# Kernel optimization log

Measured on AMD Instinct MI355X. Metric: run time of the kernel, lower is better.

## Reference

```python
import jax, jax.numpy as jnp
import numpy as np
import math

D_MODEL = 1024
NUM_HEADS = 16
D_KV = 64
INNER = NUM_HEADS * D_KV
NUM_BUCKETS = 32
MAX_DISTANCE = 128


def _relative_position_bucket(relative_position, num_buckets=NUM_BUCKETS, max_distance=MAX_DISTANCE):
    # bidirectional T5 bucketing
    n = -relative_position
    num_buckets = num_buckets // 2
    ret = (n < 0).astype(jnp.int32) * num_buckets
    n = jnp.abs(n)
    max_exact = num_buckets // 2
    is_small = n < max_exact
    n_safe = jnp.maximum(n, 1).astype(jnp.float32)  # avoid log(0); masked by is_small
    val_if_large = max_exact + (
        jnp.log(n_safe / max_exact) / math.log(max_distance / max_exact) * (num_buckets - max_exact)
    ).astype(jnp.int32)
    val_if_large = jnp.minimum(val_if_large, num_buckets - 1)
    return jnp.where(is_small, n, val_if_large) + ret


def _position_bias(rel_emb, q_len, k_len):
    ctx = jnp.arange(q_len)[:, None]
    mem = jnp.arange(k_len)[None, :]
    buckets = _relative_position_bucket(mem - ctx)          # [q, k]
    values = rel_emb[buckets]                               # [q, k, H]
    return jnp.transpose(values, (2, 0, 1))[None]           # [1, H, q, k]


def setup_inputs() -> dict:
    key = jax.random.key(0)
    ks = jax.random.split(key, 6)
    B, S = 2, 2048
    scale = 1.0 / math.sqrt(D_MODEL)
    return {
        "hidden_states": jax.random.normal(ks[0], (B, S, D_MODEL), dtype=jnp.float32),
        "mask": jnp.zeros((B, 1, 1, S), dtype=jnp.float32),
        "Wq": jax.random.normal(ks[1], (D_MODEL, INNER), dtype=jnp.float32) * scale,
        "Wk": jax.random.normal(ks[2], (D_MODEL, INNER), dtype=jnp.float32) * scale,
        "Wv": jax.random.normal(ks[3], (D_MODEL, INNER), dtype=jnp.float32) * scale,
        "Wo": jax.random.normal(ks[4], (INNER, D_MODEL), dtype=jnp.float32) * scale,
        "rel_emb": jax.random.normal(ks[5], (NUM_BUCKETS, NUM_HEADS), dtype=jnp.float32),
    }


def reference(hidden_states, mask, Wq, Wk, Wv, Wo, rel_emb):
    B, S, _ = hidden_states.shape
    def split_heads(x):
        return jnp.transpose(x.reshape(B, -1, NUM_HEADS, D_KV), (0, 2, 1, 3))  # [B,H,S,d]
    q = split_heads(hidden_states @ Wq)
    k = split_heads(hidden_states @ Wk)
    v = split_heads(hidden_states @ Wv)
    scores = jnp.einsum("bhqd,bhkd->bhqk", q, k)            # unscaled, T5-style
    position_bias = _position_bias(rel_emb, S, S)           # [1,H,S,S]
    scores = scores + position_bias + mask
    attn = jax.nn.softmax(scores, axis=-1)
    context = jnp.einsum("bhqk,bhkd->bhqd", attn, v)
    context = jnp.transpose(context, (0, 2, 1, 3)).reshape(B, S, INNER)
    output = context @ Wo
    return output, position_bias
```

## Files before the change

### kernel.cpp

```cpp
#include <hip/hip_runtime.h>
#include <cstdint>

#define AS1 __attribute__((address_space(1)))
#define AS3 __attribute__((address_space(3)))

typedef _Float16 half8 __attribute__((ext_vector_type(8)));
typedef _Float16 half4_t __attribute__((ext_vector_type(4)));
typedef float v4f __attribute__((ext_vector_type(4)));

__device__ __forceinline__ void async_ld16(const void* g, void* l) {
  __builtin_amdgcn_global_load_lds((const AS1 uint32_t*)g, (AS3 uint32_t*)l, 16, 0, 0);
}

__device__ __forceinline__ int t5_bucket(int delta) {
  int n = -delta;
  int ret = 0;
  if (n < 0) { ret = 16; n = -n; }
  if (n < 8) return n + ret;
  if (n >= 91) return 15 + ret;
  if ((n & (n - 1)) == 0) {
    int l = 31 - __clz(n);
    int v = 2 + 2 * l;
    return (v > 15 ? 15 : v) + ret;
  }
  int v = 8 + (int)(logf((float)n * 0.125f) * (8.0f / logf(16.0f)));
  return (v > 15 ? 15 : v) + ret;
}

__global__ void k_cvt(const float* __restrict__ src, _Float16* __restrict__ dst) {
  int t = blockIdx.x * 256 + threadIdx.x;
  float4 f = ((const float4*)src)[t];
  half4_t h = {(_Float16)f.x, (_Float16)f.y, (_Float16)f.z, (_Float16)f.w};
  ((half4_t*)dst)[t] = h;
}

__global__ void k_wt_all(const float* __restrict__ Wq, const float* __restrict__ Wk,
                         const float* __restrict__ Wv, const float* __restrict__ Wo,
                         _Float16* __restrict__ wqkvT, _Float16* __restrict__ woT) {
  __shared__ float tile[32][33];
  const int z = blockIdx.z;
  const float* src = (z == 0) ? Wq : (z == 1) ? Wk : (z == 2) ? Wv : Wo;
  _Float16* dst = (z < 3) ? (wqkvT + ((size_t)z << 20)) : woT;
  int tx = threadIdx.x, ty = threadIdx.y;
  int bx = blockIdx.x * 32, by = blockIdx.y * 32;
#pragma unroll
  for (int i = 0; i < 32; i += 8)
    tile[ty + i][tx] = src[(size_t)(by + ty + i) * 1024 + bx + tx];
  __syncthreads();
#pragma unroll
  for (int i = 0; i < 32; i += 8)
    dst[(size_t)(bx + ty + i) * 1024 + by + tx] = (_Float16)tile[tx][ty + i];
}

__global__ __launch_bounds__(256, 2) void k_gemm_qkv_bias(
    const _Float16* __restrict__ A, const _Float16* __restrict__ BT,
    _Float16* __restrict__ qkv, _Float16* __restrict__ vT,
    const float* __restrict__ rel, float* __restrict__ outb) {
  __shared__ __align__(16) _Float16 As[128 * 32];
  __shared__ __align__(16) _Float16 Bs[128 * 32];
  __shared__ float btab[256];
  const int tid = threadIdx.x;
  const int wave = tid >> 6, lane = tid & 63;
  const int l15 = lane & 15, quad = lane >> 4;
  const int m0 = blockIdx.y * 128, n0 = blockIdx.x * 128;
  const int wm = (wave >> 1) * 64, wn = (wave & 1) * 64;
  const int r0 = tid >> 2, c0 = (tid & 3) * 8;
  constexpr int K = 1024;

  const int bid = blockIdx.y * 24 + blockIdx.x;
  const bool do_bias = bid < 512;
  const int hB = bid >> 5;
  const int qoff = (bid & 31) * 64;
  float c_past = 0.f, c_fut = 0.f;
  if (do_bias) {
    btab[tid & 255] = rel[t5_bucket((tid & 255) - 128) * 16 + hB];
    c_past = rel[15 * 16 + hB];
    c_fut = rel[31 * 16 + hB];
  }

  v4f acc[4][4] = {};
  for (int k0 = 0; k0 < K; k0 += 32) {
    __syncthreads();
    async_ld16(A + (size_t)(m0 + r0) * K + k0 + c0, (char*)As + (size_t)(wave * 64) * 16);
    async_ld16(A + (size_t)(m0 + 64 + r0) * K + k0 + c0,
               (char*)As + (size_t)(256 + wave * 64) * 16);
    async_ld16(BT + (size_t)(n0 + r0) * K + k0 + c0, (char*)Bs + (size_t)(wave * 64) * 16);
    async_ld16(BT + (size_t)(n0 + 64 + r0) * K + k0 + c0,
               (char*)Bs + (size_t)(256 + wave * 64) * 16);
    __syncthreads();

    if (do_bias) {
      const int iter = k0 >> 5;
#pragma unroll
      for (int j = 0; j < 4; ++j) {
        int fi = iter * 1024 + j * 256 + tid;
        int qr = qoff + (fi >> 9);
        int kb = (fi & 511) * 4;
        float4 v;
        if (kb - qr >= 91) {
          v = make_float4(c_fut, c_fut, c_fut, c_fut);
        } else if (qr - kb - 3 >= 91) {
          v = make_float4(c_past, c_past, c_past, c_past);
        } else {
          v.x = btab[kb + 0 - qr + 128];
          v.y = btab[kb + 1 - qr + 128];
          v.z = btab[kb + 2 - qr + 128];
          v.w = btab[kb + 3 - qr + 128];
        }
        ((float4*)outb)[(size_t)bid * 32768 + fi] = v;
      }
    }

    half8 af[4], bf[4];
#pragma unroll
    for (int mt = 0; mt < 4; ++mt)
      af[mt] = *(const half8*)(As + (wm + mt * 16 + l15) * 32 + quad * 8);
#pragma unroll
    for (int nt = 0; nt < 4; ++nt)
      bf[nt] = *(const half8*)(Bs + (wn + nt * 16 + l15) * 32 + quad * 8);
#pragma unroll
    for (int mt = 0; mt < 4; ++mt)
#pragma unroll
      for (int nt = 0; nt < 4; ++nt)
        acc[mt][nt] = __builtin_amdgcn_mfma_f32_16x16x32_f16(af[mt], bf[nt], acc[mt][nt], 0, 0, 0);
  }
  if (n0 >= 2048) {
#pragma unroll
    for (int mt = 0; mt < 4; ++mt)
#pragma unroll
      for (int nt = 0; nt < 4; ++nt) {
        int col = n0 + wn + nt * 16 + l15 - 2048;
        int row0 = m0 + wm + mt * 16 + quad * 4;
        int bb = row0 >> 11, s0 = row0 & 2047;
        half4_t hv = {(_Float16)acc[mt][nt][0], (_Float16)acc[mt][nt][1],
                      (_Float16)acc[mt][nt][2], (_Float16)acc[mt][nt][3]};
        *(half4_t*)(vT + ((size_t)bb * 1024 + col) * 2048 + s0) = hv;
      }
    return;
  }
#pragma unroll
  for (int mt = 0; mt < 4; ++mt)
#pragma unroll
    for (int nt = 0; nt < 4; ++nt)
#pragma unroll
      for (int r = 0; r < 4; ++r)
        qkv[(size_t)(m0 + wm + mt * 16 + quad * 4 + r) * 3072 + n0 + wn + nt * 16 + l15] =
            (_Float16)acc[mt][nt][r];
}

__global__ __launch_bounds__(256, 2) void k_gemm_n64(const _Float16* __restrict__ A,
                                                     const _Float16* __restrict__ BT,
                                                     float* __restrict__ C, int K, int ldc) {
  __shared__ __align__(16) _Float16 As[128 * 32];
  __shared__ __align__(16) _Float16 Bs[64 * 32];
  const int tid = threadIdx.x;
  const int wave = tid >> 6, lane = tid & 63;
  const int l15 = lane & 15, quad = lane >> 4;
  const int m0 = blockIdx.y * 128, n0 = blockIdx.x * 64;
  const int wm = (wave >> 1) * 64, wn = (wave & 1) * 32;
  const int r0 = tid >> 2, c0 = (tid & 3) * 8;
  v4f acc[4][2] = {};
  for (int k0 = 0; k0 < K; k0 += 32) {
    __syncthreads();
    async_ld16(A + (size_t)(m0 + r0) * K + k0 + c0, (char*)As + (size_t)(wave * 64) * 16);
    async_ld16(A + (size_t)(m0 + 64 + r0) * K + k0 + c0,
               (char*)As + (size_t)(256 + wave * 64) * 16);
    async_ld16(BT + (size_t)(n0 + r0) * K + k0 + c0, (char*)Bs + (size_t)(wave * 64) * 16);
    __syncthreads();
    half8 af[4], bf[2];
#pragma unroll
    for (int mt = 0; mt < 4; ++mt)
      af[mt] = *(const half8*)(As + (wm + mt * 16 + l15) * 32 + quad * 8);
#pragma unroll
    for (int nt = 0; nt < 2; ++nt)
      bf[nt] = *(const half8*)(Bs + (wn + nt * 16 + l15) * 32 + quad * 8);
#pragma unroll
    for (int mt = 0; mt < 4; ++mt)
#pragma unroll
      for (int nt = 0; nt < 2; ++nt)
        acc[mt][nt] = __builtin_amdgcn_mfma_f32_16x16x32_f16(af[mt], bf[nt], acc[mt][nt], 0, 0, 0);
  }
#pragma unroll
  for (int mt = 0; mt < 4; ++mt)
#pragma unroll
    for (int nt = 0; nt < 2; ++nt)
#pragma unroll
      for (int r = 0; r < 4; ++r)
        C[(size_t)(m0 + wm + mt * 16 + quad * 4 + r) * ldc + n0 + wn + nt * 16 + l15] =
            acc[mt][nt][r];
}

__global__ __launch_bounds__(256, 3) void k_attn(const _Float16* __restrict__ qkv,
                                                 const _Float16* __restrict__ vT,
                                                 const float* __restrict__ mask,
                                                 const float* __restrict__ rel,
                                                 _Float16* __restrict__ ctx) {
  constexpr int S = 2048, LD = 3072;
  __shared__ __align__(16) _Float16 Ks[64 * 72];
  __shared__ __align__(16) _Float16 VT[64 * 72];
  __shared__ __align__(16) _Float16 Psh[128 * 72];
  __shared__ float btab[512];
  const int tid = threadIdx.x, wave = tid >> 6, lane = tid & 63;
  const int l15 = lane & 15, quad = lane >> 4;
  const int q0 = blockIdx.x * 128, h = blockIdx.y, b = blockIdx.z;

  for (int j = tid; j < 512; j += 256) btab[j] = rel[t5_bucket(j - 256) * 16 + h];
  const float c_past = rel[15 * 16 + h];
  const float c_fut = rel[31 * 16 + h];

  half8 bq[2][2];
#pragma unroll
  for (int qt = 0; qt < 2; ++qt) {
    const _Float16* qp = qkv + (size_t)(b * S + q0 + wave * 32 + qt * 16 + l15) * LD + h * 64;
    bq[qt][0] = *(const half8*)(qp + quad * 8);
    bq[qt][1] = *(const half8*)(qp + 32 + quad * 8);
  }
  v4f o[2][4] = {};
  float mrun[2] = {-INFINITY, -INFINITY};
  float lrun[2] = {0.f, 0.f};

  const int srow = tid >> 2, scol = (tid & 3) * 8;
  const _Float16* kg = qkv + (size_t)(b * S + srow) * LD + 1024 + h * 64 + scol;
  const _Float16* vg = vT + ((size_t)((b * 16 + h) * 64 + srow)) * S + scol;
  const float4* mkp = (const float4*)(mask + (size_t)b * S);

  for (int kv0 = 0; kv0 < S; kv0 += 64) {
    half8 kr0 = *(const half8*)(kg + (size_t)kv0 * LD);
    half8 kr1 = *(const half8*)(kg + (size_t)kv0 * LD + 32);
    half8 vr0 = *(const half8*)(vg + kv0);
    half8 vr1 = *(const half8*)(vg + kv0 + 32);
    float4 mk[4];
#pragma unroll
    for (int mt = 0; mt < 4; ++mt) mk[mt] = mkp[(kv0 >> 2) + mt * 4 + quad];
    __syncthreads();
    *(half8*)(Ks + srow * 72 + scol) = kr0;
    *(half8*)(Ks + srow * 72 + scol + 32) = kr1;
    *(half8*)(VT + srow * 72 + scol) = vr0;
    *(half8*)(VT + srow * 72 + scol + 32) = vr1;
    __syncthreads();

    v4f sc[2][4] = {};
#pragma unroll
    for (int kc = 0; kc < 2; ++kc)
#pragma unroll
      for (int mt = 0; mt < 4; ++mt) {
        half8 af = *(const half8*)(Ks + (mt * 16 + l15) * 72 + kc * 32 + quad * 8);
        sc[0][mt] = __builtin_amdgcn_mfma_f32_16x16x32_f16(af, bq[0][kc], sc[0][mt], 0, 0, 0);
        sc[1][mt] = __builtin_amdgcn_mfma_f32_16x16x32_f16(af, bq[1][kc], sc[1][mt], 0, 0, 0);
      }

    const int diff = kv0 - q0;
    const bool mixed = (diff >= -153) && (diff <= 217);
    const float cf = (diff >= 218) ? c_fut : c_past;
    v4f cm[4];
#pragma unroll
    for (int mt = 0; mt < 4; ++mt) {
      cm[mt][0] = mk[mt].x; cm[mt][1] = mk[mt].y; cm[mt][2] = mk[mt].z; cm[mt][3] = mk[mt].w;
      if (!mixed) {
        cm[mt][0] += cf; cm[mt][1] += cf; cm[mt][2] += cf; cm[mt][3] += cf;
      }
    }
    if (mixed) {
#pragma unroll
      for (int qt = 0; qt < 2; ++qt) {
        const int qq = q0 + wave * 32 + qt * 16 + l15;
#pragma unroll
        for (int mt = 0; mt < 4; ++mt) {
          int base = kv0 + mt * 16 + quad * 4 - qq + 256;
#pragma unroll
          for (int r = 0; r < 4; ++r) sc[qt][mt][r] += btab[base + r] + cm[mt][r];
        }
      }
    } else {
#pragma unroll
      for (int qt = 0; qt < 2; ++qt)
#pragma unroll
        for (int mt = 0; mt < 4; ++mt)
#pragma unroll
          for (int r = 0; r < 4; ++r) sc[qt][mt][r] += cm[mt][r];
    }

#pragma unroll
    for (int qt = 0; qt < 2; ++qt) {
      v4f m4 = sc[qt][0];
#pragma unroll
      for (int r = 0; r < 4; ++r) {
        m4[r] = fmaxf(m4[r], sc[qt][1][r]);
        m4[r] = fmaxf(m4[r], sc[qt][2][r]);
        m4[r] = fmaxf(m4[r], sc[qt][3][r]);
      }
      float mx = fmaxf(fmaxf(m4[0], m4[1]), fmaxf(m4[2], m4[3]));
      mx = fmaxf(mx, __shfl_xor(mx, 16, 64));
      mx = fmaxf(mx, __shfl_xor(mx, 32, 64));
      float mnew = fmaxf(mrun[qt], mx);
      float alpha = __expf(mrun[qt] - mnew);
      mrun[qt] = mnew;
      v4f s4 = {};
#pragma unroll
      for (int mt = 0; mt < 4; ++mt)
#pragma unroll
        for (int r = 0; r < 4; ++r) {
          float p = __expf(sc[qt][mt][r] - mnew);
          sc[qt][mt][r] = p;
          s4[r] += p;
        }
      float rs = (s4[0] + s4[1]) + (s4[2] + s4[3]);
      rs += __shfl_xor(rs, 16, 64);
      rs += __shfl_xor(rs, 32, 64);
      lrun[qt] = lrun[qt] * alpha + rs;
#pragma unroll
      for (int dt = 0; dt < 4; ++dt)
#pragma unroll
        for (int r = 0; r < 4; ++r) o[qt][dt][r] *= alpha;
      const int prow = wave * 32 + qt * 16 + l15;
#pragma unroll
      for (int mt = 0; mt < 4; ++mt) {
        half4_t ph = {(_Float16)sc[qt][mt][0], (_Float16)sc[qt][mt][1],
                      (_Float16)sc[qt][mt][2], (_Float16)sc[qt][mt][3]};
        *(half4_t*)(Psh + prow * 72 + mt * 16 + quad * 4) = ph;
      }
    }

#pragma unroll
    for (int kc = 0; kc < 2; ++kc) {
      half8 bp0 = *(const half8*)(Psh + (wave * 32 + l15) * 72 + kc * 32 + quad * 8);
      half8 bp1 = *(const half8*)(Psh + (wave * 32 + 16 + l15) * 72 + kc * 32 + quad * 8);
#pragma unroll
      for (int dt = 0; dt < 4; ++dt) {
        half8 av = *(const half8*)(VT + (dt * 16 + l15) * 72 + kc * 32 + quad * 8);
        o[0][dt] = __builtin_amdgcn_mfma_f32_16x16x32_f16(av, bp0, o[0][dt], 0, 0, 0);
        o[1][dt] = __builtin_amdgcn_mfma_f32_16x16x32_f16(av, bp1, o[1][dt], 0, 0, 0);
      }
    }
  }
#pragma unroll
  for (int qt = 0; qt < 2; ++qt) {
    float inv = 1.0f / lrun[qt];
    const size_t token = (size_t)(b * S + q0 + wave * 32 + qt * 16 + l15);
#pragma unroll
    for (int dt = 0; dt < 4; ++dt) {
      half4_t hv = {(_Float16)(o[qt][dt][0] * inv), (_Float16)(o[qt][dt][1] * inv),
                    (_Float16)(o[qt][dt][2] * inv), (_Float16)(o[qt][dt][3] * inv)};
      *(half4_t*)(ctx + token * 1024 + h * 64 + dt * 16 + quad * 4) = hv;
    }
  }
}

extern "C" void kernel_launch(void* const* d_in, const int* in_sizes, int n_in,
                              void* d_out, int out_size, void* d_ws, size_t ws_size,
                              hipStream_t stream) {
  const float* hs = (const float*)d_in[0];
  const float* mask = (const float*)d_in[1];
  const float* Wq = (const float*)d_in[2];
  const float* Wk = (const float*)d_in[3];
  const float* Wv = (const float*)d_in[4];
  const float* Wo = (const float*)d_in[5];
  const float* rel = (const float*)d_in[6];
  float* out = (float*)d_out;

  char* ws = (char*)d_ws;
  _Float16* hsF = (_Float16*)(ws);
  _Float16* wqkvT = (_Float16*)(ws + (8u << 20));
  _Float16* woT = (_Float16*)(ws + (14u << 20));
  _Float16* qkv = (_Float16*)(ws + (16u << 20));
  _Float16* ctx = (_Float16*)(ws + (40u << 20));
  _Float16* vT = (_Float16*)(ws + (48u << 20));

  k_cvt<<<4096, 256, 0, stream>>>(hs, hsF);
  k_wt_all<<<dim3(32, 32, 4), dim3(32, 8), 0, stream>>>(Wq, Wk, Wv, Wo, wqkvT, woT);

  k_gemm_qkv_bias<<<dim3(24, 32), 256, 0, stream>>>(hsF, wqkvT, qkv, vT, rel,
                                                    out + 4194304);
  k_attn<<<dim3(16, 16, 2), 256, 0, stream>>>(qkv, vT, mask, rel, ctx);
  k_gemm_n64<<<dim3(16, 32), 256, 0, stream>>>(ctx, woT, out, 1024, 1024);
}
```

Before: 435.2 us.

## Double-buffer K/V tiles in attention and merge prep kernels into one launch

```diff
diff --git a/kernel.cpp b/kernel.cpp
--- a/kernel.cpp
+++ b/kernel.cpp
@@ -27,22 +27,25 @@
   return (v > 15 ? 15 : v) + ret;
 }
 
-__global__ void k_cvt(const float* __restrict__ src, _Float16* __restrict__ dst) {
-  int t = blockIdx.x * 256 + threadIdx.x;
-  float4 f = ((const float4*)src)[t];
-  half4_t h = {(_Float16)f.x, (_Float16)f.y, (_Float16)f.z, (_Float16)f.w};
-  ((half4_t*)dst)[t] = h;
-}
-
-__global__ void k_wt_all(const float* __restrict__ Wq, const float* __restrict__ Wk,
-                         const float* __restrict__ Wv, const float* __restrict__ Wo,
-                         _Float16* __restrict__ wqkvT, _Float16* __restrict__ woT) {
+__global__ void k_prep(const float* __restrict__ hs, const float* __restrict__ Wq,
+                       const float* __restrict__ Wk, const float* __restrict__ Wv,
+                       const float* __restrict__ Wo, _Float16* __restrict__ hsF,
+                       _Float16* __restrict__ wqkvT, _Float16* __restrict__ woT) {
+  const int tid = threadIdx.x;
+  if (blockIdx.x < 4096) {
+    int t = blockIdx.x * 256 + tid;
+    float4 f = ((const float4*)hs)[t];
+    half4_t h = {(_Float16)f.x, (_Float16)f.y, (_Float16)f.z, (_Float16)f.w};
+    ((half4_t*)hsF)[t] = h;
+    return;
+  }
   __shared__ float tile[32][33];
-  const int z = blockIdx.z;
+  const int idx = blockIdx.x - 4096;
+  const int z = idx >> 10, rem = idx & 1023;
   const float* src = (z == 0) ? Wq : (z == 1) ? Wk : (z == 2) ? Wv : Wo;
   _Float16* dst = (z < 3) ? (wqkvT + ((size_t)z << 20)) : woT;
-  int tx = threadIdx.x, ty = threadIdx.y;
-  int bx = blockIdx.x * 32, by = blockIdx.y * 32;
+  const int tx = tid & 31, ty = tid >> 5;
+  const int bx = (rem & 31) * 32, by = (rem >> 5) * 32;
 #pragma unroll
   for (int i = 0; i < 32; i += 8)
     tile[ty + i][tx] = src[(size_t)(by + ty + i) * 1024 + bx + tx];
@@ -190,14 +193,14 @@
             acc[mt][nt][r];
 }
 
-__global__ __launch_bounds__(256, 3) void k_attn(const _Float16* __restrict__ qkv,
+__global__ __launch_bounds__(256, 2) void k_attn(const _Float16* __restrict__ qkv,
                                                  const _Float16* __restrict__ vT,
                                                  const float* __restrict__ mask,
                                                  const float* __restrict__ rel,
                                                  _Float16* __restrict__ ctx) {
   constexpr int S = 2048, LD = 3072;
-  __shared__ __align__(16) _Float16 Ks[64 * 72];
-  __shared__ __align__(16) _Float16 VT[64 * 72];
+  __shared__ __align__(16) _Float16 Ks[2][64 * 72];
+  __shared__ __align__(16) _Float16 VT[2][64 * 72];
   __shared__ __align__(16) _Float16 Psh[128 * 72];
   __shared__ float btab[512];
   const int tid = threadIdx.x, wave = tid >> 6, lane = tid & 63;
@@ -224,27 +227,43 @@
   const _Float16* vg = vT + ((size_t)((b * 16 + h) * 64 + srow)) * S + scol;
   const float4* mkp = (const float4*)(mask + (size_t)b * S);
 
+  {
+    half8 kr0 = *(const half8*)(kg);
+    half8 kr1 = *(const half8*)(kg + 32);
+    half8 vr0 = *(const half8*)(vg);
+    half8 vr1 = *(const half8*)(vg + 32);
+    *(half8*)(&Ks[0][srow * 72 + scol]) = kr0;
+    *(half8*)(&Ks[0][srow * 72 + scol + 32]) = kr1;
+    *(half8*)(&VT[0][srow * 72 + scol]) = vr0;
+    *(half8*)(&VT[0][srow * 72 + scol + 32]) = vr1;
+  }
+  float4 mk[4];
+#pragma unroll
+  for (int mt = 0; mt < 4; ++mt) mk[mt] = mkp[mt * 4 + quad];
+  __syncthreads();
+
   for (int kv0 = 0; kv0 < S; kv0 += 64) {
-    half8 kr0 = *(const half8*)(kg + (size_t)kv0 * LD);
-    half8 kr1 = *(const half8*)(kg + (size_t)kv0 * LD + 32);
-    half8 vr0 = *(const half8*)(vg + kv0);
-    half8 vr1 = *(const half8*)(vg + kv0 + 32);
-    float4 mk[4];
-#pragma unroll
-    for (int mt = 0; mt < 4; ++mt) mk[mt] = mkp[(kv0 >> 2) + mt * 4 + quad];
-    __syncthreads();
-    *(half8*)(Ks + srow * 72 + scol) = kr0;
-    *(half8*)(Ks + srow * 72 + scol + 32) = kr1;
-    *(half8*)(VT + srow * 72 + scol) = vr0;
-    *(half8*)(VT + srow * 72 + scol + 32) = vr1;
-    __syncthreads();
-
+    const int buf = (kv0 >> 6) & 1;
+    const bool more = (kv0 + 64) < S;
+    half8 kr0n, kr1n, vr0n, vr1n;
+    float4 mkn[4];
+    if (more) {
+      kr0n = *(const half8*)(kg + (size_t)(kv0 + 64) * LD);
+      kr1n = *(const half8*)(kg + (size_t)(kv0 + 64) * LD + 32);
+      vr0n = *(const half8*)(vg + kv0 + 64);
+      vr1n = *(const half8*)(vg + kv0 + 64 + 32);
+#pragma unroll
+      for (int mt = 0; mt < 4; ++mt) mkn[mt] = mkp[((kv0 + 64) >> 2) + mt * 4 + quad];
+    }
+
+    const _Float16* KsB = &Ks[buf][0];
+    const _Float16* VTB = &VT[buf][0];
     v4f sc[2][4] = {};
 #pragma unroll
     for (int kc = 0; kc < 2; ++kc)
 #pragma unroll
       for (int mt = 0; mt < 4; ++mt) {
-        half8 af = *(const half8*)(Ks + (mt * 16 + l15) * 72 + kc * 32 + quad * 8);
+        half8 af = *(const half8*)(KsB + (mt * 16 + l15) * 72 + kc * 32 + quad * 8);
         sc[0][mt] = __builtin_amdgcn_mfma_f32_16x16x32_f16(af, bq[0][kc], sc[0][mt], 0, 0, 0);
         sc[1][mt] = __builtin_amdgcn_mfma_f32_16x16x32_f16(af, bq[1][kc], sc[1][mt], 0, 0, 0);
       }
@@ -327,10 +346,22 @@
       half8 bp1 = *(const half8*)(Psh + (wave * 32 + 16 + l15) * 72 + kc * 32 + quad * 8);
 #pragma unroll
       for (int dt = 0; dt < 4; ++dt) {
-        half8 av = *(const half8*)(VT + (dt * 16 + l15) * 72 + kc * 32 + quad * 8);
+        half8 av = *(const half8*)(VTB + (dt * 16 + l15) * 72 + kc * 32 + quad * 8);
         o[0][dt] = __builtin_amdgcn_mfma_f32_16x16x32_f16(av, bp0, o[0][dt], 0, 0, 0);
         o[1][dt] = __builtin_amdgcn_mfma_f32_16x16x32_f16(av, bp1, o[1][dt], 0, 0, 0);
       }
+    }
+
+    if (more) {
+      _Float16* Kn = &Ks[buf ^ 1][0];
+      _Float16* Vn = &VT[buf ^ 1][0];
+      *(half8*)(Kn + srow * 72 + scol) = kr0n;
+      *(half8*)(Kn + srow * 72 + scol + 32) = kr1n;
+      *(half8*)(Vn + srow * 72 + scol) = vr0n;
+      *(half8*)(Vn + srow * 72 + scol + 32) = vr1n;
+      __syncthreads();
+#pragma unroll
+      for (int mt = 0; mt < 4; ++mt) mk[mt] = mkn[mt];
     }
   }
 #pragma unroll
@@ -366,8 +397,7 @@
   _Float16* ctx = (_Float16*)(ws + (40u << 20));
   _Float16* vT = (_Float16*)(ws + (48u << 20));
 
-  k_cvt<<<4096, 256, 0, stream>>>(hs, hsF);
-  k_wt_all<<<dim3(32, 32, 4), dim3(32, 8), 0, stream>>>(Wq, Wk, Wv, Wo, wqkvT, woT);
+  k_prep<<<8192, 256, 0, stream>>>(hs, Wq, Wk, Wv, Wo, hsF, wqkvT, woT);
 
   k_gemm_qkv_bias<<<dim3(24, 32), 256, 0, stream>>>(hsF, wqkvT, qkv, vT, rel,
                                                     out + 4194304);
```

Result: faster. 425.0 us (-2.3%).
